# Performance work log

Measured on AMD Instinct MI355X. Metric: run time of the kernel, lower is better.

## Reference

```python
import jax, jax.numpy as jnp
import numpy as np

N, C, M, K = 2, 64, 4800, 64
EPS = 1e-5  # BatchNorm eps (torch default)


def _bn_params(key, c):
    k1, k2, k3, k4 = jax.random.split(key, 4)
    g = 1.0 + 0.1 * jax.random.normal(k1, (c,), dtype=jnp.float32)
    b = 0.1 * jax.random.normal(k2, (c,), dtype=jnp.float32)
    m = 0.1 * jax.random.normal(k3, (c,), dtype=jnp.float32)
    v = jax.random.uniform(k4, (c,), dtype=jnp.float32, minval=0.5, maxval=1.5)
    return g, b, m, v


def setup_inputs() -> dict:
    key = jax.random.key(0)
    ks = jax.random.split(key, 16)
    f = lambda k, s: jax.random.normal(k, s, dtype=jnp.float32)
    g0, b0, m0, v0 = _bn_params(ks[6], C)
    g1a, b1a, m1a, v1a = _bn_params(ks[7], C)
    g1b, b1b, m1b, v1b = _bn_params(ks[8], C)
    return {
        "query_rgb_feat": f(ks[0], (N, C, M, 1)),
        "scene_rgb_feat": f(ks[1], (N, C, 1, K)),
        "scene_xyz": f(ks[2], (N, 3, 1, K)),
        "pre_xyz": f(ks[3], (N, 3, M)),
        "mask": (jax.random.uniform(ks[4], (N, 1, 1, K)) > 0.3).astype(jnp.float32),
        "W0": 0.05 * f(ks[5], (C, 2 * C)),
        "g0": g0, "b0": b0, "m0": m0, "v0": v0,
        "W1a": 0.05 * f(ks[9], (C, C + 3)),
        "g1a": g1a, "b1a": b1a, "m1a": m1a, "v1a": v1a,
        "W1b": 0.05 * f(ks[10], (C, C)),
        "g1b": g1b, "b1b": b1b, "m1b": m1b, "v1b": v1b,
        "Wskip": 0.05 * f(ks[11], (C, C + 3)),
        "Wout": 0.05 * f(ks[12], (3, C + 3)),
    }


def _conv1x1(x, W):
    # x: (N, Cin, M, K), W: (Cout, Cin) -> (N, Cout, M, K)
    return jnp.einsum('oc,ncmk->nomk', W, x)


def _bn(x, g, b, m, v):
    s = g * jax.lax.rsqrt(v + EPS)
    return x * s[None, :, None, None] + (b - m * s)[None, :, None, None]


def reference(query_rgb_feat, scene_rgb_feat, scene_xyz, pre_xyz, mask,
              W0, g0, b0, m0, v0,
              W1a, g1a, b1a, m1a, v1a,
              W1b, g1b, b1b, m1b, v1b,
              Wskip, Wout):
    n, c, m_, _ = query_rgb_feat.shape
    k_ = scene_rgb_feat.shape[-1]
    scene_feat = jnp.broadcast_to(scene_rgb_feat, (n, c, m_, k_))
    sx = scene_xyz * mask                      # (N,3,1,K) masked
    sx = jnp.broadcast_to(sx, (n, 3, m_, k_))
    q = jnp.broadcast_to(query_rgb_feat, (n, c, m_, k_))
    cat = jnp.concatenate([scene_feat, q], axis=1)            # (N,2C,M,K)
    h = jax.nn.relu(_bn(_conv1x1(cat, W0), g0, b0, m0, v0))   # fcn0
    cat2 = jnp.concatenate([h, sx], axis=1)                   # (N,C+3,M,K)
    h1 = jax.nn.relu(_bn(_conv1x1(cat2, W1a), g1a, b1a, m1a, v1a))
    h1 = jax.nn.relu(_bn(_conv1x1(h1, W1b), g1b, b1b, m1b, v1b))
    feat = h1 + _conv1x1(cat2, Wskip)                         # skip-add
    feat = jnp.max(feat, axis=-1)                             # max-pool over K -> (N,C,M)
    feat = jnp.concatenate([feat, pre_xyz], axis=1)           # (N,C+3,M)
    out = jnp.einsum('oc,ncm->nom', Wout, feat)               # out_conv -> (N,3,M)
    # torch.where(cond, out, out) in the original is a no-op; omitted.
    return out
```

## Files before the change

### kernel.cpp

```cpp
#include <hip/hip_runtime.h>

typedef unsigned int   u32;
typedef unsigned short u16;
typedef float f32x4  __attribute__((ext_vector_type(4)));
typedef short bf16x8 __attribute__((ext_vector_type(8)));
typedef u32   u32x4  __attribute__((ext_vector_type(4)));
typedef u32   u32x2  __attribute__((ext_vector_type(2)));

#define EPS 1e-5f
#define MT 4800


__device__ __forceinline__ u32 f2bf(float f) {
    union { float f; u32 i; } x; x.f = f;
    return (x.i + 0x7fffu + ((x.i >> 16) & 1u)) >> 16;
}
__device__ __forceinline__ u32 pk2(float lo, float hi) { return f2bf(lo) | (f2bf(hi) << 16); }
__device__ __forceinline__ float bflo(u32 p) { union { u32 i; float f; } x; x.i = p << 16; return x.f; }
__device__ __forceinline__ float bfhi(u32 p) { union { u32 i; float f; } x; x.i = p & 0xffff0000u; return x.f; }

union UU { u32x4 u; bf16x8 b; };

__global__ __launch_bounds__(256) void prep_w(
    const float* __restrict__ W1a, const float* __restrict__ Wsk,
    const float* __restrict__ W1b, const float* __restrict__ W0,
    u32* __restrict__ wf)
{
    int idx = blockIdx.x * 256 + threadIdx.x;
    int fi = idx >> 6, l = idx & 63;
    int g3 = fi >> 3, ct = (fi >> 1) & 3, t = fi & 1;
    int c  = ct * 16 + (l & 15);
    int j0 = t * 32 + (l >> 4) * 8;
    float v[8];
    #pragma unroll
    for (int e = 0; e < 8; ++e) {
        int j = j0 + e;
        float x;
        if      (g3 == 0) x = W1a[c * 67 + j];
        else if (g3 == 1) x = Wsk[c * 67 + j];
        else if (g3 == 2) x = W1b[c * 64 + j];
        else              x = W0[c * 128 + 64 + j];
        v[e] = x;
    }
    u32x4 p;
    p[0] = pk2(v[0], v[1]); p[1] = pk2(v[2], v[3]);
    p[2] = pk2(v[4], v[5]); p[3] = pk2(v[6], v[7]);
    ((u32x4*)wf)[idx] = p;
}

__global__ __launch_bounds__(256) void prep_nk(
    const float* __restrict__ srgb, const float* __restrict__ sxyz, const float* __restrict__ mask,
    const float* __restrict__ W0,   const float* __restrict__ W1a,  const float* __restrict__ Wsk,
    const float* __restrict__ g0, const float* __restrict__ b0, const float* __restrict__ m0_, const float* __restrict__ v0_,
    const float* __restrict__ g1a, const float* __restrict__ b1a, const float* __restrict__ m1a, const float* __restrict__ v1a,
    u16* __restrict__ stg)
{
    int idx = blockIdx.x * 256 + threadIdx.x;
    int c = idx & 63, k = (idx >> 6) & 63, n = idx >> 12;
    float dot = 0.f;
    #pragma unroll
    for (int j = 0; j < 64; ++j)
        dot += W0[c * 128 + j] * srgb[(n * 64 + j) * 64 + k];
    float s0 = g0[c] * rsqrtf(v0_[c] + EPS);
    float t0 = b0[c] - m0_[c] * s0;
    u16* base = stg + n * 13824;
    base[k * 72 + c] = (u16)f2bf(s0 * dot + t0);

    float mk = mask[n * 64 + k];
    float x0 = sxyz[(n * 3 + 0) * 64 + k] * mk;
    float x1 = sxyz[(n * 3 + 1) * 64 + k] * mk;
    float x2 = sxyz[(n * 3 + 2) * 64 + k] * mk;
    float s1a = g1a[c] * rsqrtf(v1a[c] + EPS);
    float t1a = b1a[c] - m1a[c] * s1a;
    float c1 = W1a[c * 67 + 64] * x0 + W1a[c * 67 + 65] * x1 + W1a[c * 67 + 66] * x2;
    base[4608 + c * 72 + k] = (u16)f2bf(s1a * c1 + t1a);
    float cs = Wsk[c * 67 + 64] * x0 + Wsk[c * 67 + 65] * x1 + Wsk[c * 67 + 66] * x2;
    base[9216 + c * 72 + k] = (u16)f2bf(cs);
}

__global__ __launch_bounds__(256) void ctx_mfma(
    const float* __restrict__ q, const float* __restrict__ prexyz,
    const float* __restrict__ g0, const float* __restrict__ v0_,
    const float* __restrict__ g1a, const float* __restrict__ v1a,
    const float* __restrict__ g1b, const float* __restrict__ v1b,
    const float* __restrict__ b1b, const float* __restrict__ m1b,
    const float* __restrict__ Wout,
    const u32* __restrict__ ws_u32,
    float* __restrict__ out)
{
    const int tid = threadIdx.x;
    const int w = tid >> 6, l = tid & 63;
    const int g = l >> 4, kidx = l & 15;
    const int mg = blockIdx.x, n = blockIdx.y;
    const int m0 = mg * 16;

    __shared__ u16  stage[13824];
    __shared__ u16  h1s[4][16 * 72];
    __shared__ float Bs[16 * 68];

    {
        const u32* src = ws_u32 + 8192 + n * 6912;
        u32* dst = (u32*)stage;
        #pragma unroll
        for (int j2 = 0; j2 < 27; ++j2) dst[tid + 256 * j2] = src[tid + 256 * j2];
    }

    const u32x4* wfp = (const u32x4*)ws_u32;

    bf16x8 w1a[8], wsk[8], w1b[8];
    #pragma unroll
    for (int f = 0; f < 8; ++f) { UU x; x.u = wfp[(0 * 8 + f) * 64 + l]; w1a[f] = x.b; }
    #pragma unroll
    for (int f = 0; f < 8; ++f) { UU x; x.u = wfp[(1 * 8 + f) * 64 + l]; wsk[f] = x.b; }
    #pragma unroll
    for (int f = 0; f < 8; ++f) { UU x; x.u = wfp[(2 * 8 + f) * 64 + l]; w1b[f] = x.b; }

    if (w == 0) {
        f32x4 acc0[4];
        #pragma unroll
        for (int ct = 0; ct < 4; ++ct) acc0[ct] = 0.f;
        #pragma unroll
        for (int t = 0; t < 2; ++t) {
            float qe[8];
            #pragma unroll
            for (int e = 0; e < 8; ++e)
                qe[e] = q[(n * 64 + t * 32 + g * 8 + e) * MT + m0 + kidx];
            UU a; a.u = (u32x4){pk2(qe[0], qe[1]), pk2(qe[2], qe[3]), pk2(qe[4], qe[5]), pk2(qe[6], qe[7])};
            #pragma unroll
            for (int ct = 0; ct < 4; ++ct) {
                UU wb; wb.u = wfp[(3 * 8 + ct * 2 + t) * 64 + l];
                acc0[ct] = __builtin_amdgcn_mfma_f32_16x16x32_bf16(a.b, wb.b, acc0[ct], 0, 0, 0);
            }
        }
        #pragma unroll
        for (int ct = 0; ct < 4; ++ct) {
            int c = ct * 16 + kidx;
            float s0 = g0[c] * rsqrtf(v0_[c] + EPS);
            #pragma unroll
            for (int r = 0; r < 4; ++r)
                Bs[(g * 4 + r) * 68 + c] = s0 * acc0[ct][r];
        }
    }

    float s1a_r[4], s1b_r[4], t1b_r[4], wo0[4], wo1[4], wo2[4];
    #pragma unroll
    for (int ct = 0; ct < 4; ++ct) {
        int c = ct * 16 + kidx;
        s1a_r[ct] = g1a[c] * rsqrtf(v1a[c] + EPS);
        float s1b = g1b[c] * rsqrtf(v1b[c] + EPS);
        s1b_r[ct] = s1b;
        t1b_r[ct] = b1b[c] - m1b[c] * s1b;
        wo0[ct] = Wout[0 * 67 + c];
        wo1[ct] = Wout[1 * 67 + c];
        wo2[ct] = Wout[2 * 67 + c];
    }

    __syncthreads();

    const u16* A0p = stage;
    const u16* C1p = stage + 4608;
    const u16* CSp = stage + 9216;
    u16* h1p = h1s[w];

    #pragma unroll 1
    for (int i = 0; i < 4; ++i) {
        const int m = m0 + w * 4 + i;

        float bfr[2][8];
        #pragma unroll
        for (int t = 0; t < 2; ++t)
            #pragma unroll
            for (int e = 0; e < 8; ++e)
                bfr[t][e] = Bs[(w * 4 + i) * 68 + t * 32 + g * 8 + e];

        float fmr[4];
        #pragma unroll
        for (int ct = 0; ct < 4; ++ct) fmr[ct] = -3.0e38f;

        for (int s = 0; s < 4; ++s) {
            bf16x8 af[2];
            #pragma unroll
            for (int t = 0; t < 2; ++t) {
                u32x4 a = *(const u32x4*)(A0p + (s * 16 + kidx) * 72 + t * 32 + g * 8);
                float h[8];
                h[0] = bflo(a[0]); h[1] = bfhi(a[0]); h[2] = bflo(a[1]); h[3] = bfhi(a[1]);
                h[4] = bflo(a[2]); h[5] = bfhi(a[2]); h[6] = bflo(a[3]); h[7] = bfhi(a[3]);
                #pragma unroll
                for (int e = 0; e < 8; ++e) h[e] = fmaxf(h[e] + bfr[t][e], 0.f);
                UU x; x.u = (u32x4){pk2(h[0], h[1]), pk2(h[2], h[3]), pk2(h[4], h[5]), pk2(h[6], h[7])};
                af[t] = x.b;
            }
            f32x4 acc1[4], accS[4];
            #pragma unroll
            for (int ct = 0; ct < 4; ++ct) { acc1[ct] = 0.f; accS[ct] = 0.f; }
            #pragma unroll
            for (int t = 0; t < 2; ++t)
                #pragma unroll
                for (int ct = 0; ct < 4; ++ct)
                    acc1[ct] = __builtin_amdgcn_mfma_f32_16x16x32_bf16(af[t], w1a[ct * 2 + t], acc1[ct], 0, 0, 0);
            #pragma unroll
            for (int t = 0; t < 2; ++t)
                #pragma unroll
                for (int ct = 0; ct < 4; ++ct)
                    accS[ct] = __builtin_amdgcn_mfma_f32_16x16x32_bf16(af[t], wsk[ct * 2 + t], accS[ct], 0, 0, 0);

            #pragma unroll
            for (int ct = 0; ct < 4; ++ct) {
                int c = ct * 16 + kidx;
                u32x2 cv = *(const u32x2*)(C1p + c * 72 + s * 16 + g * 4);
                float c1v[4] = {bflo(cv[0]), bfhi(cv[0]), bflo(cv[1]), bfhi(cv[1])};
                #pragma unroll
                for (int r = 0; r < 4; ++r) {
                    float h1v = fmaxf(s1a_r[ct] * acc1[ct][r] + c1v[r], 0.f);
                    h1p[(g * 4 + r) * 72 + c] = (u16)f2bf(h1v);
                }
            }
            f32x4 acc2[4];
            #pragma unroll
            for (int ct = 0; ct < 4; ++ct) acc2[ct] = 0.f;
            #pragma unroll
            for (int t = 0; t < 2; ++t) {
                UU x; x.u = *(const u32x4*)(h1p + kidx * 72 + t * 32 + g * 8);
                #pragma unroll
                for (int ct = 0; ct < 4; ++ct)
                    acc2[ct] = __builtin_amdgcn_mfma_f32_16x16x32_bf16(x.b, w1b[ct * 2 + t], acc2[ct], 0, 0, 0);
            }
            #pragma unroll
            for (int ct = 0; ct < 4; ++ct) {
                int c = ct * 16 + kidx;
                u32x2 cv = *(const u32x2*)(CSp + c * 72 + s * 16 + g * 4);
                float csv[4] = {bflo(cv[0]), bfhi(cv[0]), bflo(cv[1]), bfhi(cv[1])};
                #pragma unroll
                for (int r = 0; r < 4; ++r) {
                    float f = accS[ct][r] + csv[r] + fmaxf(s1b_r[ct] * acc2[ct][r] + t1b_r[ct], 0.f);
                    fmr[ct] = fmaxf(fmr[ct], f);
                }
            }
        }

        #pragma unroll
        for (int ct = 0; ct < 4; ++ct) {
            fmr[ct] = fmaxf(fmr[ct], __shfl_xor(fmr[ct], 16));
            fmr[ct] = fmaxf(fmr[ct], __shfl_xor(fmr[ct], 32));
        }
        float po0 = 0.f, po1 = 0.f, po2 = 0.f;
        #pragma unroll
        for (int ct = 0; ct < 4; ++ct) {
            po0 += wo0[ct] * fmr[ct];
            po1 += wo1[ct] * fmr[ct];
            po2 += wo2[ct] * fmr[ct];
        }
        #pragma unroll
        for (int d = 1; d <= 8; d <<= 1) {
            po0 += __shfl_xor(po0, d);
            po1 += __shfl_xor(po1, d);
            po2 += __shfl_xor(po2, d);
        }
        if (l < 3) {
            float p0 = prexyz[(n * 3 + 0) * MT + m];
            float p1 = prexyz[(n * 3 + 1) * MT + m];
            float p2 = prexyz[(n * 3 + 2) * MT + m];
            float o = (l == 0) ? po0 : ((l == 1) ? po1 : po2);
            o += Wout[l * 67 + 64] * p0 + Wout[l * 67 + 65] * p1 + Wout[l * 67 + 66] * p2;
            out[(n * 3 + l) * MT + m] = o;
        }
    }
}

extern "C" void kernel_launch(void* const* d_in, const int* in_sizes, int n_in,
                              void* d_out, int out_size, void* d_ws, size_t ws_size,
                              hipStream_t stream) {
    const float* q    = (const float*)d_in[0];
    const float* srgb = (const float*)d_in[1];
    const float* sxyz = (const float*)d_in[2];
    const float* pxyz = (const float*)d_in[3];
    const float* mask = (const float*)d_in[4];
    const float* W0   = (const float*)d_in[5];
    const float* g0   = (const float*)d_in[6];
    const float* b0   = (const float*)d_in[7];
    const float* m0   = (const float*)d_in[8];
    const float* v0   = (const float*)d_in[9];
    const float* W1a  = (const float*)d_in[10];
    const float* g1a  = (const float*)d_in[11];
    const float* b1a  = (const float*)d_in[12];
    const float* m1a  = (const float*)d_in[13];
    const float* v1a  = (const float*)d_in[14];
    const float* W1b  = (const float*)d_in[15];
    const float* g1b  = (const float*)d_in[16];
    const float* b1b  = (const float*)d_in[17];
    const float* m1b  = (const float*)d_in[18];
    const float* v1b  = (const float*)d_in[19];
    const float* Wsk  = (const float*)d_in[20];
    const float* Wout = (const float*)d_in[21];
    u32* ws = (u32*)d_ws;
    float* out = (float*)d_out;

    hipLaunchKernelGGL(prep_w, dim3(8), dim3(256), 0, stream, W1a, Wsk, W1b, W0, ws);
    hipLaunchKernelGGL(prep_nk, dim3(32), dim3(256), 0, stream,
        srgb, sxyz, mask, W0, W1a, Wsk,
        g0, b0, m0, v0, g1a, b1a, m1a, v1a,
        (u16*)(ws + 8192));
    hipLaunchKernelGGL(ctx_mfma, dim3(300, 2), dim3(256), 0, stream,
        q, pxyz, g0, v0, g1a, v1a, g1b, v1b, b1b, m1b, Wout, ws, out);
}
```

Before: 147.8 us.

## Fuse prep kernels into main kernel and use hardware bf16 pack conversion

Removes the two preprocessing kernels (weight packing and per-(n,k) staging) and recomputes their work inside every block of the main kernel: weights are loaded from fp32 and packed to bf16 in registers, and the scene-feature fcn0 term plus the xyz terms are computed per block with MFMA into shared memory. Software bf16 rounding is replaced by the v_cvt_pk_bf16_f32 instruction. This saves two launches and the workspace round-trip, at the cost of redundant per-block compute and extra global fp32 weight reads across 600 blocks.

Result: no change. 145.9 us (-1.3%).

```diff
diff --git a/kernel.cpp b/kernel.cpp
--- a/kernel.cpp
+++ b/kernel.cpp
@@ -10,82 +10,36 @@
 #define EPS 1e-5f
 #define MT 4800
 
-
-__device__ __forceinline__ u32 f2bf(float f) {
-    union { float f; u32 i; } x; x.f = f;
-    return (x.i + 0x7fffu + ((x.i >> 16) & 1u)) >> 16;
+__device__ __forceinline__ u32 cvtpk(float lo, float hi) {
+    u32 r;
+    asm("v_cvt_pk_bf16_f32 %0, %1, %2" : "=v"(r) : "v"(lo), "v"(hi));
+    return r;
 }
-__device__ __forceinline__ u32 pk2(float lo, float hi) { return f2bf(lo) | (f2bf(hi) << 16); }
 __device__ __forceinline__ float bflo(u32 p) { union { u32 i; float f; } x; x.i = p << 16; return x.f; }
 __device__ __forceinline__ float bfhi(u32 p) { union { u32 i; float f; } x; x.i = p & 0xffff0000u; return x.f; }
 
 union UU { u32x4 u; bf16x8 b; };
 
-__global__ __launch_bounds__(256) void prep_w(
-    const float* __restrict__ W1a, const float* __restrict__ Wsk,
-    const float* __restrict__ W1b, const float* __restrict__ W0,
-    u32* __restrict__ wf)
-{
-    int idx = blockIdx.x * 256 + threadIdx.x;
-    int fi = idx >> 6, l = idx & 63;
-    int g3 = fi >> 3, ct = (fi >> 1) & 3, t = fi & 1;
-    int c  = ct * 16 + (l & 15);
-    int j0 = t * 32 + (l >> 4) * 8;
-    float v[8];
-    #pragma unroll
-    for (int e = 0; e < 8; ++e) {
-        int j = j0 + e;
-        float x;
-        if      (g3 == 0) x = W1a[c * 67 + j];
-        else if (g3 == 1) x = Wsk[c * 67 + j];
-        else if (g3 == 2) x = W1b[c * 64 + j];
-        else              x = W0[c * 128 + 64 + j];
-        v[e] = x;
-    }
-    u32x4 p;
-    p[0] = pk2(v[0], v[1]); p[1] = pk2(v[2], v[3]);
-    p[2] = pk2(v[4], v[5]); p[3] = pk2(v[6], v[7]);
-    ((u32x4*)wf)[idx] = p;
+__device__ __forceinline__ bf16x8 pack8(const float* __restrict__ p) {
+    UU x;
+    x.u = (u32x4){cvtpk(p[0], p[1]), cvtpk(p[2], p[3]), cvtpk(p[4], p[5]), cvtpk(p[6], p[7])};
+    return x.b;
 }
 
-__global__ __launch_bounds__(256) void prep_nk(
-    const float* __restrict__ srgb, const float* __restrict__ sxyz, const float* __restrict__ mask,
-    const float* __restrict__ W0,   const float* __restrict__ W1a,  const float* __restrict__ Wsk,
-    const float* __restrict__ g0, const float* __restrict__ b0, const float* __restrict__ m0_, const float* __restrict__ v0_,
-    const float* __restrict__ g1a, const float* __restrict__ b1a, const float* __restrict__ m1a, const float* __restrict__ v1a,
-    u16* __restrict__ stg)
-{
-    int idx = blockIdx.x * 256 + threadIdx.x;
-    int c = idx & 63, k = (idx >> 6) & 63, n = idx >> 12;
-    float dot = 0.f;
-    #pragma unroll
-    for (int j = 0; j < 64; ++j)
-        dot += W0[c * 128 + j] * srgb[(n * 64 + j) * 64 + k];
-    float s0 = g0[c] * rsqrtf(v0_[c] + EPS);
-    float t0 = b0[c] - m0_[c] * s0;
-    u16* base = stg + n * 13824;
-    base[k * 72 + c] = (u16)f2bf(s0 * dot + t0);
-
-    float mk = mask[n * 64 + k];
-    float x0 = sxyz[(n * 3 + 0) * 64 + k] * mk;
-    float x1 = sxyz[(n * 3 + 1) * 64 + k] * mk;
-    float x2 = sxyz[(n * 3 + 2) * 64 + k] * mk;
-    float s1a = g1a[c] * rsqrtf(v1a[c] + EPS);
-    float t1a = b1a[c] - m1a[c] * s1a;
-    float c1 = W1a[c * 67 + 64] * x0 + W1a[c * 67 + 65] * x1 + W1a[c * 67 + 66] * x2;
-    base[4608 + c * 72 + k] = (u16)f2bf(s1a * c1 + t1a);
-    float cs = Wsk[c * 67 + 64] * x0 + Wsk[c * 67 + 65] * x1 + Wsk[c * 67 + 66] * x2;
-    base[9216 + c * 72 + k] = (u16)f2bf(cs);
-}
-
-__global__ __launch_bounds__(256) void ctx_mfma(
-    const float* __restrict__ q, const float* __restrict__ prexyz,
-    const float* __restrict__ g0, const float* __restrict__ v0_,
-    const float* __restrict__ g1a, const float* __restrict__ v1a,
-    const float* __restrict__ g1b, const float* __restrict__ v1b,
-    const float* __restrict__ b1b, const float* __restrict__ m1b,
-    const float* __restrict__ Wout,
-    const u32* __restrict__ ws_u32,
+__global__ __launch_bounds__(256) void ctx_fused(
+    const float* __restrict__ q, const float* __restrict__ srgb,
+    const float* __restrict__ sxyz, const float* __restrict__ prexyz,
+    const float* __restrict__ mask,
+    const float* __restrict__ W0,
+    const float* __restrict__ g0, const float* __restrict__ b0,
+    const float* __restrict__ m0_, const float* __restrict__ v0_,
+    const float* __restrict__ W1a,
+    const float* __restrict__ g1a, const float* __restrict__ b1a,
+    const float* __restrict__ m1a, const float* __restrict__ v1a,
+    const float* __restrict__ W1b,
+    const float* __restrict__ g1b, const float* __restrict__ b1b,
+    const float* __restrict__ m1b, const float* __restrict__ v1b,
+    const float* __restrict__ Wsk, const float* __restrict__ Wout,
     float* __restrict__ out)
 {
     const int tid = threadIdx.x;
@@ -98,22 +52,78 @@
     __shared__ u16  h1s[4][16 * 72];
     __shared__ float Bs[16 * 68];
 
-    {
-        const u32* src = ws_u32 + 8192 + n * 6912;
-        u32* dst = (u32*)stage;
-        #pragma unroll
-        for (int j2 = 0; j2 < 27; ++j2) dst[tid + 256 * j2] = src[tid + 256 * j2];
-    }
-
-    const u32x4* wfp = (const u32x4*)ws_u32;
-
     bf16x8 w1a[8], wsk[8], w1b[8];
     #pragma unroll
-    for (int f = 0; f < 8; ++f) { UU x; x.u = wfp[(0 * 8 + f) * 64 + l]; w1a[f] = x.b; }
-    #pragma unroll
-    for (int f = 0; f < 8; ++f) { UU x; x.u = wfp[(1 * 8 + f) * 64 + l]; wsk[f] = x.b; }
-    #pragma unroll
-    for (int f = 0; f < 8; ++f) { UU x; x.u = wfp[(2 * 8 + f) * 64 + l]; w1b[f] = x.b; }
+    for (int f = 0; f < 8; ++f) {
+        int ct = f >> 1, t = f & 1;
+        int c  = ct * 16 + kidx;
+        int j0 = t * 32 + g * 8;
+        w1a[f] = pack8(W1a + c * 67 + j0);
+        wsk[f] = pack8(Wsk + c * 67 + j0);
+        w1b[f] = pack8(W1b + c * 64 + j0);
+    }
+
+    {
+        f32x4 acc[4];
+        #pragma unroll
+        for (int ct = 0; ct < 4; ++ct) acc[ct] = 0.f;
+        #pragma unroll
+        for (int t = 0; t < 2; ++t) {
+            float se[8];
+            #pragma unroll
+            for (int e = 0; e < 8; ++e) {
+                int j = t * 32 + g * 8 + e;
+                se[e] = srgb[(n * 64 + j) * 64 + w * 16 + kidx];
+            }
+            UU a; a.u = (u32x4){cvtpk(se[0], se[1]), cvtpk(se[2], se[3]),
+                                cvtpk(se[4], se[5]), cvtpk(se[6], se[7])};
+            #pragma unroll
+            for (int ct = 0; ct < 4; ++ct) {
+                bf16x8 wb = pack8(W0 + (ct * 16 + kidx) * 128 + t * 32 + g * 8);
+                acc[ct] = __builtin_amdgcn_mfma_f32_16x16x32_bf16(a.b, wb, acc[ct], 0, 0, 0);
+            }
+        }
+        #pragma unroll
+        for (int ct = 0; ct < 4; ++ct) {
+            int c = ct * 16 + kidx;
+            float s0 = g0[c] * rsqrtf(v0_[c] + EPS);
+            float t0 = b0[c] - m0_[c] * s0;
+            u32 p01 = cvtpk(s0 * acc[ct][0] + t0, s0 * acc[ct][1] + t0);
+            u32 p23 = cvtpk(s0 * acc[ct][2] + t0, s0 * acc[ct][3] + t0);
+            int kb = w * 16 + g * 4;
+            stage[(kb + 0) * 72 + c] = (u16)p01;
+            stage[(kb + 1) * 72 + c] = (u16)(p01 >> 16);
+            stage[(kb + 2) * 72 + c] = (u16)p23;
+            stage[(kb + 3) * 72 + c] = (u16)(p23 >> 16);
+        }
+    }
+
+    {
+        int c  = tid & 63;
+        int kq = tid >> 6;
+        float s1a = g1a[c] * rsqrtf(v1a[c] + EPS);
+        float t1a = b1a[c] - m1a[c] * s1a;
+        float wa0 = W1a[c * 67 + 64], wa1 = W1a[c * 67 + 65], wa2 = W1a[c * 67 + 66];
+        float wsa = Wsk[c * 67 + 64], wsb = Wsk[c * 67 + 65], wsc = Wsk[c * 67 + 66];
+        u32* d1 = (u32*)(stage + 4608 + c * 72 + kq * 16);
+        u32* d2 = (u32*)(stage + 9216 + c * 72 + kq * 16);
+        #pragma unroll
+        for (int p = 0; p < 8; ++p) {
+            float v[2], s[2];
+            #pragma unroll
+            for (int h = 0; h < 2; ++h) {
+                int k = kq * 16 + p * 2 + h;
+                float mk = mask[n * 64 + k];
+                float x0 = sxyz[(n * 3 + 0) * 64 + k] * mk;
+                float x1 = sxyz[(n * 3 + 1) * 64 + k] * mk;
+                float x2 = sxyz[(n * 3 + 2) * 64 + k] * mk;
+                v[h] = s1a * (wa0 * x0 + wa1 * x1 + wa2 * x2) + t1a;
+                s[h] = wsa * x0 + wsb * x1 + wsc * x2;
+            }
+            d1[p] = cvtpk(v[0], v[1]);
+            d2[p] = cvtpk(s[0], s[1]);
+        }
+    }
 
     if (w == 0) {
         f32x4 acc0[4];
@@ -125,11 +135,12 @@
             #pragma unroll
             for (int e = 0; e < 8; ++e)
                 qe[e] = q[(n * 64 + t * 32 + g * 8 + e) * MT + m0 + kidx];
-            UU a; a.u = (u32x4){pk2(qe[0], qe[1]), pk2(qe[2], qe[3]), pk2(qe[4], qe[5]), pk2(qe[6], qe[7])};
+            UU a; a.u = (u32x4){cvtpk(qe[0], qe[1]), cvtpk(qe[2], qe[3]),
+                                cvtpk(qe[4], qe[5]), cvtpk(qe[6], qe[7])};
             #pragma unroll
             for (int ct = 0; ct < 4; ++ct) {
-                UU wb; wb.u = wfp[(3 * 8 + ct * 2 + t) * 64 + l];
-                acc0[ct] = __builtin_amdgcn_mfma_f32_16x16x32_bf16(a.b, wb.b, acc0[ct], 0, 0, 0);
+                bf16x8 wb = pack8(W0 + (ct * 16 + kidx) * 128 + 64 + t * 32 + g * 8);
+                acc0[ct] = __builtin_amdgcn_mfma_f32_16x16x32_bf16(a.b, wb, acc0[ct], 0, 0, 0);
             }
         }
         #pragma unroll
@@ -187,7 +198,8 @@
                 h[4] = bflo(a[2]); h[5] = bfhi(a[2]); h[6] = bflo(a[3]); h[7] = bfhi(a[3]);
                 #pragma unroll
                 for (int e = 0; e < 8; ++e) h[e] = fmaxf(h[e] + bfr[t][e], 0.f);
-                UU x; x.u = (u32x4){pk2(h[0], h[1]), pk2(h[2], h[3]), pk2(h[4], h[5]), pk2(h[6], h[7])};
+                UU x; x.u = (u32x4){cvtpk(h[0], h[1]), cvtpk(h[2], h[3]),
+                                    cvtpk(h[4], h[5]), cvtpk(h[6], h[7])};
                 af[t] = x.b;
             }
             f32x4 acc1[4], accS[4];
@@ -209,11 +221,16 @@
                 int c = ct * 16 + kidx;
                 u32x2 cv = *(const u32x2*)(C1p + c * 72 + s * 16 + g * 4);
                 float c1v[4] = {bflo(cv[0]), bfhi(cv[0]), bflo(cv[1]), bfhi(cv[1])};
-                #pragma unroll
-                for (int r = 0; r < 4; ++r) {
-                    float h1v = fmaxf(s1a_r[ct] * acc1[ct][r] + c1v[r], 0.f);
-                    h1p[(g * 4 + r) * 72 + c] = (u16)f2bf(h1v);
-                }
+                float hv[4];
+                #pragma unroll
+                for (int r = 0; r < 4; ++r)
+                    hv[r] = fmaxf(s1a_r[ct] * acc1[ct][r] + c1v[r], 0.f);
+                u32 p01 = cvtpk(hv[0], hv[1]);
+                u32 p23 = cvtpk(hv[2], hv[3]);
+                h1p[(g * 4 + 0) * 72 + c] = (u16)p01;
+                h1p[(g * 4 + 1) * 72 + c] = (u16)(p01 >> 16);
+                h1p[(g * 4 + 2) * 72 + c] = (u16)p23;
+                h1p[(g * 4 + 3) * 72 + c] = (u16)(p23 >> 16);
             }
             f32x4 acc2[4];
             #pragma unroll
@@ -292,14 +309,12 @@
     const float* v1b  = (const float*)d_in[19];
     const float* Wsk  = (const float*)d_in[20];
     const float* Wout = (const float*)d_in[21];
-    u32* ws = (u32*)d_ws;
     float* out = (float*)d_out;
 
-    hipLaunchKernelGGL(prep_w, dim3(8), dim3(256), 0, stream, W1a, Wsk, W1b, W0, ws);
-    hipLaunchKernelGGL(prep_nk, dim3(32), dim3(256), 0, stream,
-        srgb, sxyz, mask, W0, W1a, Wsk,
-        g0, b0, m0, v0, g1a, b1a, m1a, v1a,
-        (u16*)(ws + 8192));
-    hipLaunchKernelGGL(ctx_mfma, dim3(300, 2), dim3(256), 0, stream,
-        q, pxyz, g0, v0, g1a, v1a, g1b, v1b, b1b, m1b, Wout, ws, out);
+    hipLaunchKernelGGL(ctx_fused, dim3(300, 2), dim3(256), 0, stream,
+        q, srgb, sxyz, pxyz, mask,
+        W0, g0, b0, m0, v0,
+        W1a, g1a, b1a, m1a, v1a,
+        W1b, g1b, b1b, m1b, v1b,
+        Wsk, Wout, out);
 }
```
